# Optimization experiments

Measured on AMD Instinct MI355X. Metric: run time of the kernel, lower is better.

Reference implementation:

```python
import jax, jax.numpy as jnp
import numpy as np

SIGMA = 1.0          # influence distance of kernel points
KERNEL_RADIUS = 1.0  # radius within which kernel points live


def setup_inputs() -> dict:
    key = jax.random.key(0)
    k0, k1, k2, k3, k4 = jax.random.split(key, 5)
    B, M, K_NB, D_IN, D_OUT, K_PTS = 4, 16384, 32, 64, 64, 15
    X = jax.random.normal(k0, (B, M, 3), dtype=jnp.float32)          # point coords
    F = jax.random.normal(k1, (B, M, D_IN), dtype=jnp.float32)        # point features
    N = jax.random.randint(k2, (B, M, K_NB), 0, M)                    # neighbor indices
    Q = jax.random.uniform(k3, (K_PTS, 3), minval=-KERNEL_RADIUS,
                           maxval=KERNEL_RADIUS, dtype=jnp.float32)   # kernel points
    W = jax.random.normal(k4, (K_PTS, D_IN, D_OUT), dtype=jnp.float32) * 0.05
    return {"X": X, "F": F, "N": N, "Q": Q, "W": W}


def reference(X, F, N, Q, W):
    # Gather neighbor coordinates and features: [B, M, k, 3] / [B, M, k, d_in]
    gather = jax.vmap(lambda a, idx: a[idx])
    Xn = gather(X, N)
    Fn = gather(F, N)
    # Relative neighbor positions w.r.t. each center point
    r = Xn - X[:, :, None, :]                                  # [B, M, k, 3]
    # Distance of each relative position to each kernel point
    d = jnp.linalg.norm(r[:, :, :, None, :] - Q, axis=-1)      # [B, M, k, Kp]
    # Linear correlation influence (KPConv)
    h = jnp.maximum(0.0, 1.0 - d / SIGMA)                      # [B, M, k, Kp]
    # Distance-weighted neighbor aggregation per kernel point
    Fk = jnp.einsum('bmkp,bmkd->bmpd', h, Fn)                  # [B, M, Kp, d_in]
    # Per-kernel-point linear maps, summed over kernel points
    return jnp.einsum('bmpd,pde->bme', Fk, W)                  # [B, M, d_out]
```

## Files before the change

kernel.cpp:

```cpp
#include <hip/hip_runtime.h>
#include <hip/hip_bf16.h>


#define BATCH 4
#define MPTS  16384
#define KNB   32
#define DIN   64
#define DOUT  64
#define KP    15
#define K2P   1024
#define KSTEPS (K2P/32)
#define ROWB  (K2P*2)
#define PTS   (BATCH*MPTS)
#define PPB   32
#define NBLK  (PTS/PPB)
#define WBELEMS (K2P*DOUT)
#define WBBLK (WBELEMS/256)
#define FBBLK (PTS*DIN/8/256)
#define XPBLK (PTS/256)
#define FBOFF 131072
#define XPOFF (FBOFF + PTS*DIN*2)
#define WSNEED (XPOFF + PTS*16)

typedef __bf16 bf16x8 __attribute__((ext_vector_type(8)));
typedef float  f32x4  __attribute__((ext_vector_type(4)));
typedef unsigned short u16x8 __attribute__((ext_vector_type(8)));

static __device__ __forceinline__ unsigned short f2b(float x) {
    __bf16 h = (__bf16)x;
    return __builtin_bit_cast(unsigned short, h);
}

__global__ void prep_all(const float* __restrict__ W, const float* __restrict__ F,
                         const float* __restrict__ X,
                         unsigned short* __restrict__ wb, unsigned short* __restrict__ fb,
                         float4* __restrict__ xp, int do_xp) {
    int bid = blockIdx.x;
    if (bid < WBBLK) {
        int idx = bid * 256 + threadIdx.x;
        int i    = idx & 7;
        int lane = (idx >> 3) & 63;
        int ks   = (idx >> 9) & 31;
        int et   = idx >> 14;
        int kap  = ks * 32 + ((lane >> 4) << 3) + i;
        int n = kap >> 6;
        int g = (kap >> 4) & 3;
        int t = (kap >> 2) & 3;
        int r = kap & 3;
        int p = g * 4 + r;
        int d = n * 4 + t;
        int e = et * 16 + (lane & 15);
        float v = (p < KP) ? W[(p * DIN + d) * DOUT + e] : 0.f;
        wb[idx] = f2b(v);
    } else if (bid < WBBLK + FBBLK) {
        int i = (bid - WBBLK) * 256 + threadIdx.x;
        const float4* s = reinterpret_cast<const float4*>(F) + (size_t)i * 2;
        float4 a = s[0], b = s[1];
        u16x8 o;
        o[0] = f2b(a.x); o[1] = f2b(a.y); o[2] = f2b(a.z); o[3] = f2b(a.w);
        o[4] = f2b(b.x); o[5] = f2b(b.y); o[6] = f2b(b.z); o[7] = f2b(b.w);
        *(reinterpret_cast<u16x8*>(fb) + i) = o;
    } else if (do_xp) {
        int row = (bid - WBBLK - FBBLK) * 256 + threadIdx.x;
        const float* x = X + (size_t)row * 3;
        xp[row] = make_float4(x[0], x[1], x[2], 0.f);
    }
}

template<bool UXP>
__global__ __launch_bounds__(256, 2)
void kpconv_main(const float* __restrict__ X, const float4* __restrict__ XP,
                 const unsigned short* __restrict__ FB,
                 const int* __restrict__ NB, const float* __restrict__ Q,
                 const unsigned short* __restrict__ WB, float* __restrict__ OUT) {
    __shared__ unsigned short fk[PPB * K2P];
    __shared__ int idxs[4][8][KNB];
    char* const fkb = reinterpret_cast<char*>(fk);

    const int tid  = threadIdx.x;
    const int wv   = tid >> 6;
    const int lane = tid & 63;
    const int g16  = lane >> 4;
    const int r16  = lane & 15;

    float qx = 1.0e3f, qy = 0.f, qz = 0.f;
    if (r16 < KP) { qx = Q[r16 * 3 + 0]; qy = Q[r16 * 3 + 1]; qz = Q[r16 * 3 + 2]; }
    const float qq   = qx * qx + qy * qy + qz * qz;
    const float nq2x = -2.f * qx, nq2y = -2.f * qy, nq2z = -2.f * qz;

    const int bid     = blockIdx.x;
    const int base_pt = (bid & 7) * (PTS / 8) + (bid >> 3) * PPB;
    const int boff    = (base_pt >> 14) * MPTS;
    const int pid0    = base_pt + wv * 8;

    #pragma unroll
    for (int e = 0; e < 4; ++e) {
        int ent = lane + e * 64;
        int j = ent >> 5, k = ent & 31;
        int pid = pid0 + j;
        int nb  = NB[(size_t)pid * KNB + k];
        int gidx = boff + nb;
        float rx, ry, rz;
        if constexpr (UXP) {
            float4 xn = XP[gidx];
            float4 xc = XP[pid];
            rx = xn.x - xc.x; ry = xn.y - xc.y; rz = xn.z - xc.z;
        } else {
            const float* xn = X + (size_t)gidx * 3;
            const float* xc = X + (size_t)pid * 3;
            rx = xn[0] - xc[0]; ry = xn[1] - xc[1]; rz = xn[2] - xc[2];
        }
        float rr = fmaf(rx, rx, fmaf(ry, ry, rz * rz));
        int slot = (k & 24) | ((k ^ (k >> 3)) & 7);
        *reinterpret_cast<float4*>(fkb + (wv * 8 + j) * ROWB + slot * 16) =
            make_float4(rx, ry, rz, rr);
        idxs[wv][j][k] = gidx;
    }

    union U { uint2 d; unsigned short s[4]; };
    U L[2][8];

    auto issue_gather = [&](int j, U* Lj) {
        const int4* ip = reinterpret_cast<const int4*>(&idxs[wv][j][g16 * 8]);
        int4 a = ip[0];
        int4 b = ip[1];
        int g[8] = {a.x, a.y, a.z, a.w, b.x, b.y, b.z, b.w};
        #pragma unroll
        for (int i = 0; i < 8; ++i)
            Lj[i].d = *reinterpret_cast<const uint2*>(
                FB + ((size_t)g[i] << 6) + (r16 << 2));
    };

    issue_gather(0, L[0]);
    issue_gather(1, L[1]);

    #pragma unroll
    for (int j = 0; j < 8; ++j) {
        const int row = wv * 8 + j;

        bf16x8 ah;
        #pragma unroll
        for (int i = 0; i < 8; ++i) {
            float4 rv = *reinterpret_cast<const float4*>(
                fkb + row * ROWB + (g16 * 8 + (i ^ g16)) * 16);
            float d2 = fmaf(rv.x, nq2x, fmaf(rv.y, nq2y, fmaf(rv.z, nq2z, rv.w + qq)));
            d2 = fmaxf(d2, 0.f);
            ah[i] = (__bf16)fmaxf(1.f - __builtin_amdgcn_sqrtf(d2), 0.f);
        }

        bf16x8 bfr[4];
        #pragma unroll
        for (int t = 0; t < 4; ++t)
            #pragma unroll
            for (int i = 0; i < 8; ++i)
                bfr[t][i] = __builtin_bit_cast(__bf16, L[j & 1][i].s[t]);

        if (j < 6) issue_gather(j + 2, L[j & 1]);

        const f32x4 z = {0.f, 0.f, 0.f, 0.f};
        f32x4 accs[4];
        #pragma unroll
        for (int t = 0; t < 4; ++t)
            accs[t] = __builtin_amdgcn_mfma_f32_16x16x32_bf16(ah, bfr[t], z, 0, 0, 0);

        bf16x8 w0, w1;
        #pragma unroll
        for (int r = 0; r < 4; ++r) {
            w0[r]     = (__bf16)accs[0][r];
            w0[4 + r] = (__bf16)accs[1][r];
            w1[r]     = (__bf16)accs[2][r];
            w1[4 + r] = (__bf16)accs[3][r];
        }
        int swz  = (row & 7) ^ (r16 & 7);
        int off0 = row * ROWB + (r16 * 8 + ((g16 * 2 + 0) ^ swz)) * 16;
        int off1 = row * ROWB + (r16 * 8 + ((g16 * 2 + 1) ^ swz)) * 16;
        *reinterpret_cast<bf16x8*>(fkb + off0) = w0;
        *reinterpret_cast<bf16x8*>(fkb + off1) = w1;
    }

    __syncthreads();

    const unsigned short* wbp = WB + ((size_t)(wv * KSTEPS) * 64 + lane) * 8;
    asm volatile("" : "+v"(wbp));

    f32x4 o0 = {0.f, 0.f, 0.f, 0.f};
    f32x4 o1 = {0.f, 0.f, 0.f, 0.f};
    #pragma unroll
    for (int ks = 0; ks < KSTEPS; ++ks) {
        bf16x8 b = *reinterpret_cast<const bf16x8*>(wbp + ks * 512);
        int stored = (ks * 4 + g16) ^ (r16 & 7) ^ ((ks >> 1) & 7);
        bf16x8 a0 = *reinterpret_cast<const bf16x8*>(fkb + r16 * ROWB + stored * 16);
        bf16x8 a1 = *reinterpret_cast<const bf16x8*>(fkb + (16 + r16) * ROWB + stored * 16);
        o0 = __builtin_amdgcn_mfma_f32_16x16x32_bf16(a0, b, o0, 0, 0, 0);
        o1 = __builtin_amdgcn_mfma_f32_16x16x32_bf16(a1, b, o1, 0, 0, 0);
    }

    #pragma unroll
    for (int r = 0; r < 4; ++r) {
        int p0 = base_pt + g16 * 4 + r;
        OUT[(size_t)p0 * DOUT + wv * 16 + r16] = o0[r];
        int p1 = base_pt + 16 + g16 * 4 + r;
        OUT[(size_t)p1 * DOUT + wv * 16 + r16] = o1[r];
    }
}

extern "C" void kernel_launch(void* const* d_in, const int* in_sizes, int n_in,
                              void* d_out, int out_size, void* d_ws, size_t ws_size,
                              hipStream_t stream) {
    const float* X = (const float*)d_in[0];
    const float* F = (const float*)d_in[1];
    const int*   N = (const int*)d_in[2];
    const float* Q = (const float*)d_in[3];
    const float* W = (const float*)d_in[4];
    float* OUT = (float*)d_out;
    unsigned short* WB = (unsigned short*)d_ws;
    unsigned short* FB = (unsigned short*)((char*)d_ws + FBOFF);
    float4*         XP = (float4*)((char*)d_ws + XPOFF);

    const int use_xp = (ws_size >= (size_t)WSNEED) ? 1 : 0;

    prep_all<<<WBBLK + FBBLK + (use_xp ? XPBLK : 0), 256, 0, stream>>>(
        W, F, X, WB, FB, XP, use_xp);

    if (use_xp)
        kpconv_main<true><<<NBLK, 256, 0, stream>>>(X, XP, FB, N, Q, WB, OUT);
    else
        kpconv_main<false><<<NBLK, 256, 0, stream>>>(X, XP, FB, N, Q, WB, OUT);
}
```

Measured before the change: 55.07 us.

## Skip feature gathers for neighbors outside all kernel-point influence radii

Computes all influence weights before the gather loop and uses a wave ballot to find neighbors whose distance to every kernel point is at least sigma. Those neighbors get all-zero weights, so their gathers are redirected to one shared row (boff), which turns scattered loads into cache hits. It also prefetches the first four weight fragments of the second GEMM before the block barrier. The cost is extra registers to hold eight precomputed weight vectors, which may lower occupancy. Correctness holds because the skipped rows are multiplied by zero weights.

```diff
diff --git a/kernel.cpp b/kernel.cpp
--- a/kernel.cpp
+++ b/kernel.cpp
@@ -117,36 +117,50 @@
         idxs[wv][j][k] = gidx;
     }
 
+    bf16x8 ah[8];
+    int    act[8];
+    #pragma unroll
+    for (int j = 0; j < 8; ++j) {
+        const int row = wv * 8 + j;
+        bf16x8 a;
+        int am = 0;
+        #pragma unroll
+        for (int i = 0; i < 8; ++i) {
+            float4 rv = *reinterpret_cast<const float4*>(
+                fkb + row * ROWB + (g16 * 8 + (i ^ g16)) * 16);
+            float d2 = fmaf(rv.x, nq2x, fmaf(rv.y, nq2y, fmaf(rv.z, nq2z, rv.w + qq)));
+            unsigned long long m = __ballot(d2 < 1.0f);
+            unsigned grp = (unsigned)(m >> (g16 * 16)) & 0xffffu;
+            am |= (grp ? 1 : 0) << i;
+            d2 = fmaxf(d2, 0.f);
+            a[i] = (__bf16)fmaxf(1.f - __builtin_amdgcn_sqrtf(d2), 0.f);
+        }
+        ah[j]  = a;
+        act[j] = am;
+    }
+
     union U { uint2 d; unsigned short s[4]; };
     U L[2][8];
 
-    auto issue_gather = [&](int j, U* Lj) {
+    auto issue_gather = [&](int j, U* Lj, int am) {
         const int4* ip = reinterpret_cast<const int4*>(&idxs[wv][j][g16 * 8]);
         int4 a = ip[0];
         int4 b = ip[1];
         int g[8] = {a.x, a.y, a.z, a.w, b.x, b.y, b.z, b.w};
         #pragma unroll
-        for (int i = 0; i < 8; ++i)
+        for (int i = 0; i < 8; ++i) {
+            int gi = ((am >> i) & 1) ? g[i] : boff;
             Lj[i].d = *reinterpret_cast<const uint2*>(
-                FB + ((size_t)g[i] << 6) + (r16 << 2));
+                FB + ((size_t)gi << 6) + (r16 << 2));
+        }
     };
 
-    issue_gather(0, L[0]);
-    issue_gather(1, L[1]);
+    issue_gather(0, L[0], act[0]);
+    issue_gather(1, L[1], act[1]);
 
     #pragma unroll
     for (int j = 0; j < 8; ++j) {
         const int row = wv * 8 + j;
-
-        bf16x8 ah;
-        #pragma unroll
-        for (int i = 0; i < 8; ++i) {
-            float4 rv = *reinterpret_cast<const float4*>(
-                fkb + row * ROWB + (g16 * 8 + (i ^ g16)) * 16);
-            float d2 = fmaf(rv.x, nq2x, fmaf(rv.y, nq2y, fmaf(rv.z, nq2z, rv.w + qq)));
-            d2 = fmaxf(d2, 0.f);
-            ah[i] = (__bf16)fmaxf(1.f - __builtin_amdgcn_sqrtf(d2), 0.f);
-        }
 
         bf16x8 bfr[4];
         #pragma unroll
@@ -155,13 +169,13 @@
             for (int i = 0; i < 8; ++i)
                 bfr[t][i] = __builtin_bit_cast(__bf16, L[j & 1][i].s[t]);
 
-        if (j < 6) issue_gather(j + 2, L[j & 1]);
+        if (j < 6) issue_gather(j + 2, L[j & 1], act[j + 2]);
 
         const f32x4 z = {0.f, 0.f, 0.f, 0.f};
         f32x4 accs[4];
         #pragma unroll
         for (int t = 0; t < 4; ++t)
-            accs[t] = __builtin_amdgcn_mfma_f32_16x16x32_bf16(ah, bfr[t], z, 0, 0, 0);
+            accs[t] = __builtin_amdgcn_mfma_f32_16x16x32_bf16(ah[j], bfr[t], z, 0, 0, 0);
 
         bf16x8 w0, w1;
         #pragma unroll
@@ -178,16 +192,21 @@
         *reinterpret_cast<bf16x8*>(fkb + off1) = w1;
     }
 
-    __syncthreads();
-
     const unsigned short* wbp = WB + ((size_t)(wv * KSTEPS) * 64 + lane) * 8;
     asm volatile("" : "+v"(wbp));
+    bf16x8 bpre[4];
+    #pragma unroll
+    for (int t = 0; t < 4; ++t)
+        bpre[t] = *reinterpret_cast<const bf16x8*>(wbp + t * 512);
+
+    __syncthreads();
 
     f32x4 o0 = {0.f, 0.f, 0.f, 0.f};
     f32x4 o1 = {0.f, 0.f, 0.f, 0.f};
     #pragma unroll
     for (int ks = 0; ks < KSTEPS; ++ks) {
-        bf16x8 b = *reinterpret_cast<const bf16x8*>(wbp + ks * 512);
+        bf16x8 b = (ks < 4) ? bpre[ks]
+                            : *reinterpret_cast<const bf16x8*>(wbp + ks * 512);
         int stored = (ks * 4 + g16) ^ (r16 & 7) ^ ((ks >> 1) & 7);
         bf16x8 a0 = *reinterpret_cast<const bf16x8*>(fkb + r16 * ROWB + stored * 16);
         bf16x8 a1 = *reinterpret_cast<const bf16x8*>(fkb + (16 + r16) * ROWB + stored * 16);
```

Result: slower. 58.79 us (+6.8%).
